# Kernel optimization log

Measured on AMD Instinct MI355X. Metric: run time of the kernel, lower is better.

## Reference

```python
import jax, jax.numpy as jnp
import numpy as np

B, T, M, DK, DV, S = 64, 256, 64, 128, 256, 128
NSK, NQ = 200, 2000


def _glorot(k, shape):
    lim = np.sqrt(6.0 / (shape[0] + shape[1])).astype(np.float32)
    return jax.random.uniform(k, shape, jnp.float32, -lim, lim)


def setup_inputs() -> dict:
    key = jax.random.key(0)
    ks = jax.random.split(key, 16)
    tn = lambda k, shape: 0.1 * jax.random.truncated_normal(k, -2.0, 2.0, shape, jnp.float32)
    return {
        "q_data": jax.random.randint(ks[0], (B, T), 0, NSK + 1),
        "qa_data": jax.random.randint(ks[1], (B, T), 0, 2 * NSK + 1),
        "s_data": jax.random.randint(ks[2], (B, T), 0, NQ + 1),
        "key_memory": tn(ks[3], (M, DK)),
        "value_memory": tn(ks[4], (M, DV)),
        "Eq": 0.05 * jax.random.normal(ks[5], (NSK + 1, DK), jnp.float32),
        "Eqa": 0.05 * jax.random.normal(ks[6], (2 * NSK + 1, DV), jnp.float32),
        "Es": 0.05 * jax.random.normal(ks[7], (NQ + 1, DK), jnp.float32),
        "We": _glorot(ks[8], (DV, DV)), "be": jnp.zeros((DV,), jnp.float32),
        "Wa": _glorot(ks[9], (DV, DV)), "ba": jnp.zeros((DV,), jnp.float32),
        "Wsa": _glorot(ks[10], (DV, M)), "bsa": jnp.zeros((M,), jnp.float32),
        "Wqd1": _glorot(ks[11], (DK, S)), "bqd1": jnp.zeros((S,), jnp.float32),
        "Wqd": _glorot(ks[12], (S, 1)), "bqd": jnp.zeros((1,), jnp.float32),
        "Wsd1": _glorot(ks[13], (DK, S)), "bsd1": jnp.zeros((S,), jnp.float32),
        "Wsd": _glorot(ks[14], (S, 1)), "bsd": jnp.zeros((1,), jnp.float32),
    }


def reference(q_data, qa_data, s_data, key_memory, value_memory, Eq, Eqa, Es,
              We, be, Wa, ba, Wsa, bsa, Wqd1, bqd1, Wqd, bqd, Wsd1, bsd1, Wsd, bsd):
    b = q_data.shape[0]
    qe = Eq[q_data]    # [B,T,DK]
    qae = Eqa[qa_data]  # [B,T,DV]
    se = Es[s_data]    # [B,T,DK]
    # time-independent precomputation (same math, hoisted out of the loop)
    corr = jax.nn.softmax(jnp.einsum("btk,mk->btm", qe, key_memory), axis=-1)  # [B,T,M]
    erase = qae @ We + be  # [B,T,DV] (activation=None in source)
    add = qae @ Wa + ba    # [B,T,DV]
    qd = jnp.tanh(qe @ Wqd1 + bqd1) @ Wqd + bqd  # [B,T,1]
    sd = jnp.tanh(se @ Wsd1 + bsd1) @ Wsd + bsd  # [B,T,1]

    def step(Mv, x):
        cw, er, ad = x  # [B,M], [B,DV], [B,DV]
        read = jnp.einsum("bm,bmd->bd", cw, Mv)        # read BEFORE write
        sa1 = read @ Wsa + bsa                          # [B,M]
        sa = jnp.sum(cw * sa1, axis=1)                  # [B]
        scale = cw[:, :, None]                          # [B,M,1]
        Mv_new = Mv * (1.0 - er[:, None, :] * scale) + ad[:, None, :] * scale
        return Mv_new, sa

    Mv0 = jnp.broadcast_to(value_memory[None], (b,) + value_memory.shape)
    xs = (corr.transpose(1, 0, 2), erase.transpose(1, 0, 2), add.transpose(1, 0, 2))
    _, sa_t = jax.lax.scan(step, Mv0, xs)  # sa_t: [T,B]
    z = 3.0 * sa_t.T - qd[..., 0] - sd[..., 0]  # [B,T]
    return jax.nn.sigmoid(z)
```

## Files before the change

### kernel.cpp

```cpp
#include <hip/hip_runtime.h>
#include <math.h>

#define B_   64
#define T_   256
#define M_   64
#define DK_  128
#define DV_  256
#define S_   128
#define NQR  201
#define NQAR 401
#define NSR  2001

typedef float f2 __attribute__((ext_vector_type(2)));

static __device__ __forceinline__ int imin(int a, int b){ return a < b ? a : b; }

static __device__ __forceinline__ float fast_tanh(float x){
  float e = __expf(2.f * x);
  return 1.f - 2.f / (e + 1.f);
}

template<int CTRL, int RM>
static __device__ __forceinline__ float dppadd(float x) {
  return x + __int_as_float(
      __builtin_amdgcn_update_dpp(0, __float_as_int(x), CTRL, RM, 0xf, true));
}
static __device__ __forceinline__ float wave_sum_lane63(float x) {
  x = dppadd<0x111, 0xf>(x);
  x = dppadd<0x112, 0xf>(x);
  x = dppadd<0x114, 0xf>(x);
  x = dppadd<0x118, 0xf>(x);
  x = dppadd<0x142, 0xa>(x);
  x = dppadd<0x143, 0xc>(x);
  return x;
}
static __device__ __forceinline__ float half_sum_lane31_63(float x) {
  x = dppadd<0x111, 0xf>(x);
  x = dppadd<0x112, 0xf>(x);
  x = dppadd<0x114, 0xf>(x);
  x = dppadd<0x118, 0xf>(x);
  x = dppadd<0x142, 0xa>(x);
  return x;
}

__device__ void corr_role(int blk, const float* __restrict__ Eq,
                          const float* __restrict__ Km,
                          const float* __restrict__ Wsa,
                          const float* __restrict__ bsa,
                          float* __restrict__ corr,
                          float* __restrict__ w2_t,
                          float* __restrict__ csb_t)
{
  __shared__ float eq[4][DK_];
  __shared__ float cwb[4][M_];
  const int w = threadIdx.x >> 6, m = threadIdx.x & 63;
  const int i  = blk * 4 + w;
  const int ic = imin(i, NQR - 1);
  eq[w][m]      = Eq[ic * DK_ + m];
  eq[w][m + 64] = Eq[ic * DK_ + 64 + m];
  float acc = 0.f;
  const float4* kr = (const float4*)(Km + m * DK_);
  #pragma unroll 8
  for (int k4 = 0; k4 < DK_ / 4; ++k4) {
    float4 kv = kr[k4];
    acc = fmaf(eq[w][k4 * 4 + 0], kv.x, acc);
    acc = fmaf(eq[w][k4 * 4 + 1], kv.y, acc);
    acc = fmaf(eq[w][k4 * 4 + 2], kv.z, acc);
    acc = fmaf(eq[w][k4 * 4 + 3], kv.w, acc);
  }
  float mx = acc;
  #pragma unroll
  for (int off = 32; off; off >>= 1) mx = fmaxf(mx, __shfl_xor(mx, off, 64));
  float e = __expf(acc - mx);
  float ssum = e;
  #pragma unroll
  for (int off = 32; off; off >>= 1) ssum += __shfl_xor(ssum, off, 64);
  const float cw = e / ssum;
  if (i < NQR) corr[i * M_ + m] = cw;
  cwb[w][m] = cw;

  float pv = wave_sum_lane63(cw * bsa[m]);
  if (m == 63 && i < NQR) csb_t[i] = pv;

  float aw[4] = {0,0,0,0};
  for (int mm4 = 0; mm4 < M_ / 4; ++mm4) {
    #pragma unroll
    for (int r = 0; r < 4; ++r) {
      float4 wv = *(const float4*)(Wsa + (r * 64 + m) * M_ + mm4 * 4);
      aw[r] = fmaf(cwb[w][mm4 * 4 + 0], wv.x, aw[r]);
      aw[r] = fmaf(cwb[w][mm4 * 4 + 1], wv.y, aw[r]);
      aw[r] = fmaf(cwb[w][mm4 * 4 + 2], wv.z, aw[r]);
      aw[r] = fmaf(cwb[w][mm4 * 4 + 3], wv.w, aw[r]);
    }
  }
  if (i < NQR) {
    #pragma unroll
    for (int r = 0; r < 4; ++r) w2_t[i * DV_ + r * 64 + m] = aw[r];
  }
}

__device__ void ea_role(int blk, const float* __restrict__ Eqa,
                        const float* __restrict__ We, const float* __restrict__ be,
                        const float* __restrict__ Wa, const float* __restrict__ ba,
                        float* __restrict__ eat)
{
  __shared__ float a[8][DV_];
  const int d  = threadIdx.x;
  const int i0 = blk * 8;
  #pragma unroll
  for (int r = 0; r < 8; ++r) a[r][d] = Eqa[imin(i0 + r, NQAR - 1) * DV_ + d];
  __syncthreads();
  float er[8] = {0,0,0,0,0,0,0,0}, ad[8] = {0,0,0,0,0,0,0,0};
  for (int k = 0; k < DV_; ++k) {
    float we = We[k * DV_ + d];
    float wa = Wa[k * DV_ + d];
    #pragma unroll
    for (int r = 0; r < 8; ++r) {
      er[r] = fmaf(a[r][k], we, er[r]);
      ad[r] = fmaf(a[r][k], wa, ad[r]);
    }
  }
  const float beo = be[d], bao = ba[d];
  #pragma unroll
  for (int r = 0; r < 8; ++r) {
    int i = i0 + r;
    if (i < NQAR) {
      float2 v; v.x = er[r] + beo; v.y = ad[r] + bao;
      *(float2*)(eat + (size_t)(i * DV_ + d) * 2) = v;
    }
  }
}

__device__ void mlp_role(int blk, const float* __restrict__ E,
                         const float* __restrict__ W1, const float* __restrict__ b1,
                         const float* __restrict__ W2v, const float* __restrict__ b2,
                         float* __restrict__ outt, int nrows)
{
  __shared__ float e[8 * S_];
  __shared__ float red[8][2];
  const int tid = threadIdx.x;
  const int s = tid & 127, rh = tid >> 7;
  const int i0 = blk * 8;
  #pragma unroll
  for (int j = 0; j < 4; ++j) {
    int x = tid + j * 256;
    int row = imin(i0 + (x >> 7), nrows - 1);
    e[x] = E[row * DK_ + (x & 127)];
  }
  __syncthreads();
  float acc[4] = {0,0,0,0};
  const float* eb = e + rh * 4 * 128;
  for (int k = 0; k < DK_; ++k) {
    float wv = W1[k * S_ + s];
    #pragma unroll
    for (int r = 0; r < 4; ++r) acc[r] = fmaf(eb[r * 128 + k], wv, acc[r]);
  }
  const float b1s = b1[s], w2s = W2v[s];
  float p[4];
  #pragma unroll
  for (int r = 0; r < 4; ++r) p[r] = fast_tanh(acc[r] + b1s) * w2s;
  #pragma unroll
  for (int r = 0; r < 4; ++r) p[r] = wave_sum_lane63(p[r]);
  const int lane = tid & 63;
  const int half = s >> 6;
  if (lane == 63) {
    #pragma unroll
    for (int r = 0; r < 4; ++r) red[rh * 4 + r][half] = p[r];
  }
  __syncthreads();
  if (tid < 8) {
    int i = i0 + tid;
    if (i < nrows) outt[i] = red[tid][0] + red[tid][1] + b2[0];
  }
}

__device__ void pk_role(int blk, const int* __restrict__ q,
                        const int* __restrict__ qa, int* __restrict__ pkt)
{
  const int i = (blk * 256 + threadIdx.x) * 4;
  int4 qv = *(const int4*)(q + i);
  int4 av = *(const int4*)(qa + i);
  int4 p;
  p.x = (av.x << 16) | qv.x;
  p.y = (av.y << 16) | qv.y;
  p.z = (av.z << 16) | qv.z;
  p.w = (av.w << 16) | qv.w;
  *(int4*)(pkt + i) = p;
}

#define NB_CORR 51
#define NB_EA   51
#define NB_QD   26
#define NB_SD   251
#define NB_PK   16
#define NB_TOT  (NB_CORR + NB_EA + NB_QD + NB_SD + NB_PK)

__global__ __launch_bounds__(256) void tables_kernel(
    const int* q_data, const int* qa_data, int* pkt,
    const float* Eq, const float* Km, const float* Wsa, const float* bsa,
    float* corr_t, float* w2_t, float* csb_t,
    const float* Eqa, const float* We, const float* be,
    const float* Wa, const float* ba, float* eat,
    const float* Wqd1, const float* bqd1, const float* Wqd, const float* bqd, float* qd_t,
    const float* Es, const float* Wsd1, const float* bsd1, const float* Wsd, const float* bsd, float* sd_t)
{
  int blk = blockIdx.x;
  if (blk < NB_CORR) { corr_role(blk, Eq, Km, Wsa, bsa, corr_t, w2_t, csb_t); return; }
  blk -= NB_CORR;
  if (blk < NB_EA)   { ea_role(blk, Eqa, We, be, Wa, ba, eat); return; }
  blk -= NB_EA;
  if (blk < NB_QD)   { mlp_role(blk, Eq, Wqd1, bqd1, Wqd, bqd, qd_t, NQR); return; }
  blk -= NB_QD;
  if (blk < NB_SD)   { mlp_role(blk, Es, Wsd1, bsd1, Wsd, bsd, sd_t, NSR); return; }
  blk -= NB_SD;
  pk_role(blk, q_data, qa_data, pkt);
}

static __device__ __forceinline__ int4 getpk(const int4& pk, int g) {
  int4 r;
  r.x = __builtin_amdgcn_readlane(pk.x, g);
  r.y = __builtin_amdgcn_readlane(pk.y, g);
  r.z = __builtin_amdgcn_readlane(pk.z, g);
  r.w = __builtin_amdgcn_readlane(pk.w, g);
  return r;
}
#define PQ(v)  ((v) & 0xffff)
#define PA(v)  ((int)(((unsigned)(v)) >> 16))

static __device__ __forceinline__ float stepp(
    f2& Mv01, f2& Mv23, f2& Mv45, f2& Mv67,
    f2 c01, f2 c23, f2 c45, f2 c67, f2 ea, float w2)
{
  f2 er2; er2.x = ea.x; er2.y = ea.x;
  f2 ad2; ad2.x = ea.y; ad2.y = ea.y;
  f2 r = c01 * Mv01;
  f2 t0 = __builtin_elementwise_fma(er2, -Mv01, ad2);
  Mv01 = __builtin_elementwise_fma(c01, t0, Mv01);
  r = __builtin_elementwise_fma(c23, Mv23, r);
  f2 t1 = __builtin_elementwise_fma(er2, -Mv23, ad2);
  Mv23 = __builtin_elementwise_fma(c23, t1, Mv23);
  r = __builtin_elementwise_fma(c45, Mv45, r);
  f2 t2 = __builtin_elementwise_fma(er2, -Mv45, ad2);
  Mv45 = __builtin_elementwise_fma(c45, t2, Mv45);
  r = __builtin_elementwise_fma(c67, Mv67, r);
  f2 t3 = __builtin_elementwise_fma(er2, -Mv67, ad2);
  Mv67 = __builtin_elementwise_fma(c67, t3, Mv67);
  return (r.x + r.y) * w2;
}

#define FETCH_C(P) do { \
  const f2* _p0 = (const f2*)(corr_t + PQ((P).x) * M_ + m0); \
  const f2* _p1 = (const f2*)(corr_t + PQ((P).y) * M_ + m0); \
  const f2* _p2 = (const f2*)(corr_t + PQ((P).z) * M_ + m0); \
  const f2* _p3 = (const f2*)(corr_t + PQ((P).w) * M_ + m0); \
  c0_01=_p0[0]; c0_23=_p0[1]; c0_45=_p0[2]; c0_67=_p0[3]; \
  c1_01=_p1[0]; c1_23=_p1[1]; c1_45=_p1[2]; c1_67=_p1[3]; \
  c2_01=_p2[0]; c2_23=_p2[1]; c2_45=_p2[2]; c2_67=_p2[3]; \
  c3_01=_p3[0]; c3_23=_p3[1]; c3_45=_p3[2]; c3_67=_p3[3]; \
} while(0)

#define FETCH_V(P, ea0,ea1,ea2,ea3, w0,w1,w2v,w3) do { \
  ea0 = *(const f2*)(eat + (size_t)(PA((P).x) * DV_ + d) * 2); \
  ea1 = *(const f2*)(eat + (size_t)(PA((P).y) * DV_ + d) * 2); \
  ea2 = *(const f2*)(eat + (size_t)(PA((P).z) * DV_ + d) * 2); \
  ea3 = *(const f2*)(eat + (size_t)(PA((P).w) * DV_ + d) * 2); \
  w0  = w2_t[PQ((P).x) * DV_ + d]; \
  w1  = w2_t[PQ((P).y) * DV_ + d]; \
  w2v = w2_t[PQ((P).z) * DV_ + d]; \
  w3  = w2_t[PQ((P).w) * DV_ + d]; \
} while(0)

__global__ __launch_bounds__(512) void scan_kernel(
    const int* __restrict__ pkt,
    const float* __restrict__ corr_t, const float* __restrict__ eat,
    const float* __restrict__ w2_t,
    const float* __restrict__ Vm, float* __restrict__ sa_part)
{
  const int b   = blockIdx.y;
  const int dq  = blockIdx.x;
  const int tid = threadIdx.x;
  const int dl  = tid & 63;
  const int mg  = tid >> 6;
  const int m0  = __builtin_amdgcn_readfirstlane(mg * 8);
  const int d   = dq * 64 + dl;
  const int half = dl >> 5;

  const int4 pk = ((const int4*)(pkt + b * T_))[dl];

  f2 Mv01, Mv23, Mv45, Mv67;
  Mv01.x = Vm[(m0 + 0) * DV_ + d];  Mv01.y = Vm[(m0 + 1) * DV_ + d];
  Mv23.x = Vm[(m0 + 2) * DV_ + d];  Mv23.y = Vm[(m0 + 3) * DV_ + d];
  Mv45.x = Vm[(m0 + 4) * DV_ + d];  Mv45.y = Vm[(m0 + 5) * DV_ + d];
  Mv67.x = Vm[(m0 + 6) * DV_ + d];  Mv67.y = Vm[(m0 + 7) * DV_ + d];

  float* baseP = sa_part + ((dq * 16 + mg * 2 + half) * B_ + b) * T_;

  f2 c0_01, c0_23, c0_45, c0_67;
  f2 c1_01, c1_23, c1_45, c1_67;
  f2 c2_01, c2_23, c2_45, c2_67;
  f2 c3_01, c3_23, c3_45, c3_67;
  f2 eE0, eE1, eE2, eE3, eO0, eO1, eO2, eO3;
  float wE0, wE1, wE2, wE3, wO0, wO1, wO2, wO3;

  int4 I0 = getpk(pk, 0);
  int4 I1 = getpk(pk, 1);
  FETCH_C(I0);
  FETCH_V(I0, eE0,eE1,eE2,eE3, wE0,wE1,wE2,wE3);
  FETCH_V(I1, eO0,eO1,eO2,eO3, wO0,wO1,wO2,wO3);
  int4 Icur = I1;
  int4 Inxt = getpk(pk, 2);

  for (int g = 0; g < 64; g += 2) {
    float s0 = stepp(Mv01,Mv23,Mv45,Mv67, c0_01,c0_23,c0_45,c0_67, eE0, wE0);
    float s1 = stepp(Mv01,Mv23,Mv45,Mv67, c1_01,c1_23,c1_45,c1_67, eE1, wE1);
    float s2 = stepp(Mv01,Mv23,Mv45,Mv67, c2_01,c2_23,c2_45,c2_67, eE2, wE2);
    float s3 = stepp(Mv01,Mv23,Mv45,Mv67, c3_01,c3_23,c3_45,c3_67, eE3, wE3);
    FETCH_C(Icur);
    FETCH_V(Inxt, eE0,eE1,eE2,eE3, wE0,wE1,wE2,wE3);
    Icur = Inxt;
    Inxt = getpk(pk, (g + 3) & 63);
    float4 p;
    p.x = half_sum_lane31_63(s0);
    p.y = half_sum_lane31_63(s1);
    p.z = half_sum_lane31_63(s2);
    p.w = half_sum_lane31_63(s3);
    if ((dl & 31) == 31) *(float4*)(baseP + 4 * g) = p;

    s0 = stepp(Mv01,Mv23,Mv45,Mv67, c0_01,c0_23,c0_45,c0_67, eO0, wO0);
    s1 = stepp(Mv01,Mv23,Mv45,Mv67, c1_01,c1_23,c1_45,c1_67, eO1, wO1);
    s2 = stepp(Mv01,Mv23,Mv45,Mv67, c2_01,c2_23,c2_45,c2_67, eO2, wO2);
    s3 = stepp(Mv01,Mv23,Mv45,Mv67, c3_01,c3_23,c3_45,c3_67, eO3, wO3);
    FETCH_C(Icur);
    FETCH_V(Inxt, eO0,eO1,eO2,eO3, wO0,wO1,wO2,wO3);
    Icur = Inxt;
    Inxt = getpk(pk, (g + 4) & 63);
    p.x = half_sum_lane31_63(s0);
    p.y = half_sum_lane31_63(s1);
    p.z = half_sum_lane31_63(s2);
    p.w = half_sum_lane31_63(s3);
    if ((dl & 31) == 31) *(float4*)(baseP + 4 * g + 4) = p;
  }
}

__global__ __launch_bounds__(256) void final_kernel(
    const int* __restrict__ q_data, const int* __restrict__ s_data,
    const float* __restrict__ sa_part, const float* __restrict__ csb_t,
    const float* __restrict__ qd_t, const float* __restrict__ sd_t,
    float* __restrict__ out)
{
  const int b = blockIdx.x, t = threadIdx.x;
  float s = 0.f;
  #pragma unroll
  for (int p = 0; p < 64; ++p) s += sa_part[(p * B_ + b) * T_ + t];
  const int bt = b * T_ + t;
  const int q  = q_data[bt];
  const int si = s_data[bt];
  const float sa = s + csb_t[q];
  const float z = 3.f * sa - qd_t[q] - sd_t[si];
  out[bt] = 1.f / (1.f + __expf(-z));
}

extern "C" void kernel_launch(void* const* d_in, const int* in_sizes, int n_in,
                              void* d_out, int out_size, void* d_ws, size_t ws_size,
                              hipStream_t stream)
{
  const int*   q_data = (const int*)d_in[0];
  const int*   qa_data= (const int*)d_in[1];
  const int*   s_data = (const int*)d_in[2];
  const float* Km     = (const float*)d_in[3];
  const float* Vm     = (const float*)d_in[4];
  const float* Eq     = (const float*)d_in[5];
  const float* Eqa    = (const float*)d_in[6];
  const float* Es     = (const float*)d_in[7];
  const float* We     = (const float*)d_in[8];
  const float* be     = (const float*)d_in[9];
  const float* Wa     = (const float*)d_in[10];
  const float* ba     = (const float*)d_in[11];
  const float* Wsa    = (const float*)d_in[12];
  const float* bsa    = (const float*)d_in[13];
  const float* Wqd1   = (const float*)d_in[14];
  const float* bqd1   = (const float*)d_in[15];
  const float* Wqd    = (const float*)d_in[16];
  const float* bqd    = (const float*)d_in[17];
  const float* Wsd1   = (const float*)d_in[18];
  const float* bsd1   = (const float*)d_in[19];
  const float* Wsd    = (const float*)d_in[20];
  const float* bsd    = (const float*)d_in[21];
  float* out = (float*)d_out;

  float* wsf    = (float*)d_ws;
  float* corr_t = wsf;
  float* w2_t   = corr_t + NQR * M_;
  float* csb_t  = w2_t + NQR * DV_;
  float* eat    = csb_t + 204;
  float* qd_t   = eat + NQAR * DV_ * 2;
  float* sd_t   = qd_t + 204;
  int*   pkt    = (int*)(sd_t + 2004);
  float* sa_p   = sd_t + 2004 + 16384;

  tables_kernel<<<NB_TOT, 256, 0, stream>>>(
      q_data, qa_data, pkt,
      Eq, Km, Wsa, bsa, corr_t, w2_t, csb_t,
      Eqa, We, be, Wa, ba, eat,
      Wqd1, bqd1, Wqd, bqd, qd_t,
      Es, Wsd1, bsd1, Wsd, bsd, sd_t);
  scan_kernel<<<dim3(4, B_), 512, 0, stream>>>(pkt, corr_t, eat, w2_t, Vm, sa_p);
  final_kernel<<<B_, 256, 0, stream>>>(q_data, s_data, sa_p, csb_t, qd_t, sd_t, out);
}
```

Before: 159.3 us.

## Split scan memory rows across twice as many blocks and pre-broadcast erase/add table

The scan kernel now launches 8 blocks per batch row instead of 4, and each thread keeps 4 memory slots instead of 8. This halves the serial FMA chain per time step and doubles the number of waves available to hide gather latency. The per-step partial sums now use a full 64-lane DPP reduction rather than two 32-lane halves, so the number of partial-sum slots stays the same. The erase/add table is written as a pre-duplicated float4 so the scan loads ready-made vector pairs without shuffling. In exchange, the table is twice as large, and each thread spends more corr/eat/w2 gather traffic and reduction work relative to its arithmetic.

New measurement: 181.0 us. 13.6% more time.

```diff
diff --git a/kernel.cpp b/kernel.cpp
--- a/kernel.cpp
+++ b/kernel.cpp
@@ -32,14 +32,6 @@
   x = dppadd<0x118, 0xf>(x);
   x = dppadd<0x142, 0xa>(x);
   x = dppadd<0x143, 0xc>(x);
-  return x;
-}
-static __device__ __forceinline__ float half_sum_lane31_63(float x) {
-  x = dppadd<0x111, 0xf>(x);
-  x = dppadd<0x112, 0xf>(x);
-  x = dppadd<0x114, 0xf>(x);
-  x = dppadd<0x118, 0xf>(x);
-  x = dppadd<0x142, 0xa>(x);
   return x;
 }
 
@@ -102,7 +94,7 @@
 __device__ void ea_role(int blk, const float* __restrict__ Eqa,
                         const float* __restrict__ We, const float* __restrict__ be,
                         const float* __restrict__ Wa, const float* __restrict__ ba,
-                        float* __restrict__ eat)
+                        float* __restrict__ eat2)
 {
   __shared__ float a[8][DV_];
   const int d  = threadIdx.x;
@@ -125,8 +117,10 @@
   for (int r = 0; r < 8; ++r) {
     int i = i0 + r;
     if (i < NQAR) {
-      float2 v; v.x = er[r] + beo; v.y = ad[r] + bao;
-      *(float2*)(eat + (size_t)(i * DV_ + d) * 2) = v;
+      float4 v;
+      v.x = er[r] + beo;  v.y = v.x;
+      v.z = ad[r] + bao;  v.w = v.z;
+      *(float4*)(eat2 + (size_t)(i * DV_ + d) * 4) = v;
     }
   }
 }
@@ -200,14 +194,14 @@
     const float* Eq, const float* Km, const float* Wsa, const float* bsa,
     float* corr_t, float* w2_t, float* csb_t,
     const float* Eqa, const float* We, const float* be,
-    const float* Wa, const float* ba, float* eat,
+    const float* Wa, const float* ba, float* eat2,
     const float* Wqd1, const float* bqd1, const float* Wqd, const float* bqd, float* qd_t,
     const float* Es, const float* Wsd1, const float* bsd1, const float* Wsd, const float* bsd, float* sd_t)
 {
   int blk = blockIdx.x;
   if (blk < NB_CORR) { corr_role(blk, Eq, Km, Wsa, bsa, corr_t, w2_t, csb_t); return; }
   blk -= NB_CORR;
-  if (blk < NB_EA)   { ea_role(blk, Eqa, We, be, Wa, ba, eat); return; }
+  if (blk < NB_EA)   { ea_role(blk, Eqa, We, be, Wa, ba, eat2); return; }
   blk -= NB_EA;
   if (blk < NB_QD)   { mlp_role(blk, Eq, Wqd1, bqd1, Wqd, bqd, qd_t, NQR); return; }
   blk -= NB_QD;
@@ -228,23 +222,14 @@
 #define PA(v)  ((int)(((unsigned)(v)) >> 16))
 
 static __device__ __forceinline__ float stepp(
-    f2& Mv01, f2& Mv23, f2& Mv45, f2& Mv67,
-    f2 c01, f2 c23, f2 c45, f2 c67, f2 ea, float w2)
-{
-  f2 er2; er2.x = ea.x; er2.y = ea.x;
-  f2 ad2; ad2.x = ea.y; ad2.y = ea.y;
+    f2& Mv01, f2& Mv23, f2 c01, f2 c23, f2 er2, f2 ad2, float w2)
+{
   f2 r = c01 * Mv01;
   f2 t0 = __builtin_elementwise_fma(er2, -Mv01, ad2);
   Mv01 = __builtin_elementwise_fma(c01, t0, Mv01);
   r = __builtin_elementwise_fma(c23, Mv23, r);
   f2 t1 = __builtin_elementwise_fma(er2, -Mv23, ad2);
   Mv23 = __builtin_elementwise_fma(c23, t1, Mv23);
-  r = __builtin_elementwise_fma(c45, Mv45, r);
-  f2 t2 = __builtin_elementwise_fma(er2, -Mv45, ad2);
-  Mv45 = __builtin_elementwise_fma(c45, t2, Mv45);
-  r = __builtin_elementwise_fma(c67, Mv67, r);
-  f2 t3 = __builtin_elementwise_fma(er2, -Mv67, ad2);
-  Mv67 = __builtin_elementwise_fma(c67, t3, Mv67);
   return (r.x + r.y) * w2;
 }
 
@@ -253,17 +238,21 @@
   const f2* _p1 = (const f2*)(corr_t + PQ((P).y) * M_ + m0); \
   const f2* _p2 = (const f2*)(corr_t + PQ((P).z) * M_ + m0); \
   const f2* _p3 = (const f2*)(corr_t + PQ((P).w) * M_ + m0); \
-  c0_01=_p0[0]; c0_23=_p0[1]; c0_45=_p0[2]; c0_67=_p0[3]; \
-  c1_01=_p1[0]; c1_23=_p1[1]; c1_45=_p1[2]; c1_67=_p1[3]; \
-  c2_01=_p2[0]; c2_23=_p2[1]; c2_45=_p2[2]; c2_67=_p2[3]; \
-  c3_01=_p3[0]; c3_23=_p3[1]; c3_45=_p3[2]; c3_67=_p3[3]; \
+  c0_01=_p0[0]; c0_23=_p0[1]; \
+  c1_01=_p1[0]; c1_23=_p1[1]; \
+  c2_01=_p2[0]; c2_23=_p2[1]; \
+  c3_01=_p3[0]; c3_23=_p3[1]; \
 } while(0)
 
-#define FETCH_V(P, ea0,ea1,ea2,ea3, w0,w1,w2v,w3) do { \
-  ea0 = *(const f2*)(eat + (size_t)(PA((P).x) * DV_ + d) * 2); \
-  ea1 = *(const f2*)(eat + (size_t)(PA((P).y) * DV_ + d) * 2); \
-  ea2 = *(const f2*)(eat + (size_t)(PA((P).z) * DV_ + d) * 2); \
-  ea3 = *(const f2*)(eat + (size_t)(PA((P).w) * DV_ + d) * 2); \
+#define FETCH_V(P, e0,a0,e1,a1,e2,a2,e3,a3, w0,w1,w2v,w3) do { \
+  float4 _v0 = *(const float4*)(eat2 + (size_t)(PA((P).x) * DV_ + d) * 4); \
+  float4 _v1 = *(const float4*)(eat2 + (size_t)(PA((P).y) * DV_ + d) * 4); \
+  float4 _v2 = *(const float4*)(eat2 + (size_t)(PA((P).z) * DV_ + d) * 4); \
+  float4 _v3 = *(const float4*)(eat2 + (size_t)(PA((P).w) * DV_ + d) * 4); \
+  e0.x=_v0.x; e0.y=_v0.y; a0.x=_v0.z; a0.y=_v0.w; \
+  e1.x=_v1.x; e1.y=_v1.y; a1.x=_v1.z; a1.y=_v1.w; \
+  e2.x=_v2.x; e2.y=_v2.y; a2.x=_v2.z; a2.y=_v2.w; \
+  e3.x=_v3.x; e3.y=_v3.y; a3.x=_v3.z; a3.y=_v3.w; \
   w0  = w2_t[PQ((P).x) * DV_ + d]; \
   w1  = w2_t[PQ((P).y) * DV_ + d]; \
   w2v = w2_t[PQ((P).z) * DV_ + d]; \
@@ -272,73 +261,71 @@
 
 __global__ __launch_bounds__(512) void scan_kernel(
     const int* __restrict__ pkt,
-    const float* __restrict__ corr_t, const float* __restrict__ eat,
+    const float* __restrict__ corr_t, const float* __restrict__ eat2,
     const float* __restrict__ w2_t,
     const float* __restrict__ Vm, float* __restrict__ sa_part)
 {
   const int b   = blockIdx.y;
-  const int dq  = blockIdx.x;
+  const int x   = blockIdx.x;
+  const int dq  = x >> 1;
+  const int mh  = x & 1;
   const int tid = threadIdx.x;
   const int dl  = tid & 63;
-  const int mg  = tid >> 6;
-  const int m0  = __builtin_amdgcn_readfirstlane(mg * 8);
+  const int w   = tid >> 6;
+  const int mg  = mh * 8 + w;
+  const int m0  = __builtin_amdgcn_readfirstlane(mg * 4);
   const int d   = dq * 64 + dl;
-  const int half = dl >> 5;
 
   const int4 pk = ((const int4*)(pkt + b * T_))[dl];
 
-  f2 Mv01, Mv23, Mv45, Mv67;
+  f2 Mv01, Mv23;
   Mv01.x = Vm[(m0 + 0) * DV_ + d];  Mv01.y = Vm[(m0 + 1) * DV_ + d];
   Mv23.x = Vm[(m0 + 2) * DV_ + d];  Mv23.y = Vm[(m0 + 3) * DV_ + d];
-  Mv45.x = Vm[(m0 + 4) * DV_ + d];  Mv45.y = Vm[(m0 + 5) * DV_ + d];
-  Mv67.x = Vm[(m0 + 6) * DV_ + d];  Mv67.y = Vm[(m0 + 7) * DV_ + d];
-
-  float* baseP = sa_part + ((dq * 16 + mg * 2 + half) * B_ + b) * T_;
-
-  f2 c0_01, c0_23, c0_45, c0_67;
-  f2 c1_01, c1_23, c1_45, c1_67;
-  f2 c2_01, c2_23, c2_45, c2_67;
-  f2 c3_01, c3_23, c3_45, c3_67;
-  f2 eE0, eE1, eE2, eE3, eO0, eO1, eO2, eO3;
+
+  float* baseP = sa_part + ((dq * 16 + mg) * B_ + b) * T_;
+
+  f2 c0_01, c0_23, c1_01, c1_23, c2_01, c2_23, c3_01, c3_23;
+  f2 eE0, aE0, eE1, aE1, eE2, aE2, eE3, aE3;
+  f2 eO0, aO0, eO1, aO1, eO2, aO2, eO3, aO3;
   float wE0, wE1, wE2, wE3, wO0, wO1, wO2, wO3;
 
   int4 I0 = getpk(pk, 0);
   int4 I1 = getpk(pk, 1);
   FETCH_C(I0);
-  FETCH_V(I0, eE0,eE1,eE2,eE3, wE0,wE1,wE2,wE3);
-  FETCH_V(I1, eO0,eO1,eO2,eO3, wO0,wO1,wO2,wO3);
+  FETCH_V(I0, eE0,aE0,eE1,aE1,eE2,aE2,eE3,aE3, wE0,wE1,wE2,wE3);
+  FETCH_V(I1, eO0,aO0,eO1,aO1,eO2,aO2,eO3,aO3, wO0,wO1,wO2,wO3);
   int4 Icur = I1;
   int4 Inxt = getpk(pk, 2);
 
   for (int g = 0; g < 64; g += 2) {
-    float s0 = stepp(Mv01,Mv23,Mv45,Mv67, c0_01,c0_23,c0_45,c0_67, eE0, wE0);
-    float s1 = stepp(Mv01,Mv23,Mv45,Mv67, c1_01,c1_23,c1_45,c1_67, eE1, wE1);
-    float s2 = stepp(Mv01,Mv23,Mv45,Mv67, c2_01,c2_23,c2_45,c2_67, eE2, wE2);
-    float s3 = stepp(Mv01,Mv23,Mv45,Mv67, c3_01,c3_23,c3_45,c3_67, eE3, wE3);
+    float s0 = stepp(Mv01, Mv23, c0_01, c0_23, eE0, aE0, wE0);
+    float s1 = stepp(Mv01, Mv23, c1_01, c1_23, eE1, aE1, wE1);
+    float s2 = stepp(Mv01, Mv23, c2_01, c2_23, eE2, aE2, wE2);
+    float s3 = stepp(Mv01, Mv23, c3_01, c3_23, eE3, aE3, wE3);
     FETCH_C(Icur);
-    FETCH_V(Inxt, eE0,eE1,eE2,eE3, wE0,wE1,wE2,wE3);
+    FETCH_V(Inxt, eE0,aE0,eE1,aE1,eE2,aE2,eE3,aE3, wE0,wE1,wE2,wE3);
     Icur = Inxt;
     Inxt = getpk(pk, (g + 3) & 63);
     float4 p;
-    p.x = half_sum_lane31_63(s0);
-    p.y = half_sum_lane31_63(s1);
-    p.z = half_sum_lane31_63(s2);
-    p.w = half_sum_lane31_63(s3);
-    if ((dl & 31) == 31) *(float4*)(baseP + 4 * g) = p;
-
-    s0 = stepp(Mv01,Mv23,Mv45,Mv67, c0_01,c0_23,c0_45,c0_67, eO0, wO0);
-    s1 = stepp(Mv01,Mv23,Mv45,Mv67, c1_01,c1_23,c1_45,c1_67, eO1, wO1);
-    s2 = stepp(Mv01,Mv23,Mv45,Mv67, c2_01,c2_23,c2_45,c2_67, eO2, wO2);
-    s3 = stepp(Mv01,Mv23,Mv45,Mv67, c3_01,c3_23,c3_45,c3_67, eO3, wO3);
+    p.x = wave_sum_lane63(s0);
+    p.y = wave_sum_lane63(s1);
+    p.z = wave_sum_lane63(s2);
+    p.w = wave_sum_lane63(s3);
+    if (dl == 63) *(float4*)(baseP + 4 * g) = p;
+
+    s0 = stepp(Mv01, Mv23, c0_01, c0_23, eO0, aO0, wO0);
+    s1 = stepp(Mv01, Mv23, c1_01, c1_23, eO1, aO1, wO1);
+    s2 = stepp(Mv01, Mv23, c2_01, c2_23, eO2, aO2, wO2);
+    s3 = stepp(Mv01, Mv23, c3_01, c3_23, eO3, aO3, wO3);
     FETCH_C(Icur);
-    FETCH_V(Inxt, eO0,eO1,eO2,eO3, wO0,wO1,wO2,wO3);
+    FETCH_V(Inxt, eO0,aO0,eO1,aO1,eO2,aO2,eO3,aO3, wO0,wO1,wO2,wO3);
     Icur = Inxt;
     Inxt = getpk(pk, (g + 4) & 63);
-    p.x = half_sum_lane31_63(s0);
-    p.y = half_sum_lane31_63(s1);
-    p.z = half_sum_lane31_63(s2);
-    p.w = half_sum_lane31_63(s3);
-    if ((dl & 31) == 31) *(float4*)(baseP + 4 * g + 4) = p;
+    p.x = wave_sum_lane63(s0);
+    p.y = wave_sum_lane63(s1);
+    p.z = wave_sum_lane63(s2);
+    p.w = wave_sum_lane63(s3);
+    if (dl == 63) *(float4*)(baseP + 4 * g + 4) = p;
   }
 }
 
@@ -392,8 +379,8 @@
   float* corr_t = wsf;
   float* w2_t   = corr_t + NQR * M_;
   float* csb_t  = w2_t + NQR * DV_;
-  float* eat    = csb_t + 204;
-  float* qd_t   = eat + NQAR * DV_ * 2;
+  float* eat2   = csb_t + 204;
+  float* qd_t   = eat2 + NQAR * DV_ * 4;
   float* sd_t   = qd_t + 204;
   int*   pkt    = (int*)(sd_t + 2004);
   float* sa_p   = sd_t + 2004 + 16384;
@@ -401,9 +388,9 @@
   tables_kernel<<<NB_TOT, 256, 0, stream>>>(
       q_data, qa_data, pkt,
       Eq, Km, Wsa, bsa, corr_t, w2_t, csb_t,
-      Eqa, We, be, Wa, ba, eat,
+      Eqa, We, be, Wa, ba, eat2,
       Wqd1, bqd1, Wqd, bqd, qd_t,
       Es, Wsd1, bsd1, Wsd, bsd, sd_t);
-  scan_kernel<<<dim3(4, B_), 512, 0, stream>>>(pkt, corr_t, eat, w2_t, Vm, sa_p);
+  scan_kernel<<<dim3(8, B_), 512, 0, stream>>>(pkt, corr_t, eat2, w2_t, Vm, sa_p);
   final_kernel<<<B_, 256, 0, stream>>>(q_data, s_data, sa_p, csb_t, qd_t, sd_t, out);
 }
```
